# Kernel optimization log

Measured on AMD Instinct MI355X. Metric: run time of the kernel, lower is better.

The kernel has to match this reference:

```python
import jax, jax.numpy as jnp
import numpy as np
from jax import lax


def _maxpool_same(x, k):
    # stride-1 max pool with symmetric padding p=(k-1)//2, pad value -inf
    # (matches torch max_pool2d implicit -inf padding)
    p = (k - 1) // 2
    return lax.reduce_window(
        x,
        -jnp.inf,
        lax.max,
        window_dimensions=(1, 1, k, k),
        window_strides=(1, 1, 1, 1),
        padding=[(0, 0), (0, 0), (p, p), (p, p)],
    )


def setup_inputs() -> dict:
    key = jax.random.key(0)
    x = jax.random.normal(key, (16, 256, 64, 64), dtype=jnp.float32)
    return {"x": x}


def reference(x):
    # SPP: concat(x, maxpool5(x), maxpool9(x), maxpool13(x)) along channels
    x1 = _maxpool_same(x, 5)
    x2 = _maxpool_same(x, 9)
    x3 = _maxpool_same(x, 13)
    return jnp.concatenate([x, x1, x2, x3], axis=1)  # [B, 4C, H, W]
```

## Files before the change

### kernel.cpp

```cpp
#include <hip/hip_runtime.h>
#include <math.h>

#define TPB 256
#define W 64
#define H 64
#define LDSW 68

typedef float f32x4 __attribute__((ext_vector_type(4)));

__device__ __forceinline__ f32x4 max4(f32x4 a, f32x4 b) {
    f32x4 r;
    r.x = fmaxf(a.x, b.x); r.y = fmaxf(a.y, b.y);
    r.z = fmaxf(a.z, b.z); r.w = fmaxf(a.w, b.w);
    return r;
}

__device__ __forceinline__ void lds_barrier() {
    asm volatile("s_waitcnt lgkmcnt(0)\n\ts_barrier" ::: "memory");
}

__device__ __forceinline__ void p1_rest(const f32x4 v[4], float* __restrict__ s,
                                        float* __restrict__ outimg, int tid) {
    const int  lane = tid & 63;
    const int  lm1 = (lane - 1) & 63;
    const int  lp1 = (lane + 1) & 63;
    const bool qlo = (lane & 15) == 0;
    const bool qhi = (lane & 15) == 15;
    const float NEG = -INFINITY;
    f32x4* o4 = (f32x4*)outimg;
    #pragma unroll
    for (int i = 0; i < 4; ++i) {
        const int idx = tid + TPB * i;
        f32x4 t = v[i];
        __builtin_nontemporal_store(t, o4 + idx);
        float e0 = __shfl(t.z, lm1, 64);
        float e1 = __shfl(t.w, lm1, 64);
        float e6 = __shfl(t.x, lp1, 64);
        float e7 = __shfl(t.y, lp1, 64);
        if (qlo) { e0 = NEG; e1 = NEG; }
        if (qhi) { e6 = NEG; e7 = NEG; }
        const float e2 = t.x, e3 = t.y, e4 = t.z, e5 = t.w;
        const float p0 = fmaxf(e0, e1), p1 = fmaxf(e1, e2), p2 = fmaxf(e2, e3);
        const float p3 = fmaxf(e3, e4), p4 = fmaxf(e4, e5), p5 = fmaxf(e5, e6);
        f32x4 r;
        r.x = fmaxf(fmaxf(p0, p2), e4);
        r.y = fmaxf(fmaxf(p1, p3), e5);
        r.z = fmaxf(fmaxf(p2, p4), e6);
        r.w = fmaxf(fmaxf(p3, p5), e7);
        const int y = idx >> 4;
        const int q = idx & 15;
        *(f32x4*)&s[y * LDSW + 4 * q] = r;
    }
}

__device__ __forceinline__ void p2(const float* __restrict__ s,
                                   float* __restrict__ outimg, int tid) {
    const float NEG = -INFINITY;
    const size_t pstr = (size_t)256 * H * W;
    const int g    = tid & 15;
    const int x0   = g << 2;
    const int y0   = (tid >> 4) << 2;
    const int lane = tid & 63;
    const int lm1  = (lane - 1) & 63;
    const int lp1  = (lane + 1) & 63;
    const bool qlo = (g == 0);
    const bool qhi = (g == 15);

    f32x4 cv[16];
    #pragma unroll
    for (int j = 0; j < 16; ++j) {
        const int y  = y0 - 6 + j;
        const int yc = y < 0 ? 0 : (y > 63 ? 63 : y);
        f32x4 v = *(const f32x4*)&s[yc * LDSW + x0];
        if (y < 0 || y > 63) v = (f32x4){NEG, NEG, NEG, NEG};
        cv[j] = v;
    }
    f32x4 m2[15], m4[13], m8[9];
    #pragma unroll
    for (int j = 0; j < 15; ++j) m2[j] = max4(cv[j], cv[j + 1]);
    #pragma unroll
    for (int j = 0; j < 13; ++j) m4[j] = max4(m2[j], m2[j + 2]);
    #pragma unroll
    for (int j = 0; j < 9;  ++j) m8[j] = max4(m4[j], m4[j + 4]);

    float* o5  = outimg +     pstr;
    float* o9  = outimg + 2 * pstr;
    float* o13 = outimg + 3 * pstr;
    #pragma unroll
    for (int i = 0; i < 4; ++i) {
        const f32x4 c5  = max4(m4[i + 4], cv[i + 8]);
        const f32x4 c9  = max4(m8[i + 2], cv[i + 10]);
        const f32x4 c13 = max4(max4(m8[i], m4[i + 8]), cv[i + 12]);

        __builtin_nontemporal_store(c5, (f32x4*)(o5 + (y0 + i) * W + x0));

        const float Lz = __shfl(c9.z, lm1, 64);
        const float Lw = __shfl(c9.w, lm1, 64);
        const float Rx = __shfl(c9.x, lp1, 64);
        const float Ry = __shfl(c9.y, lp1, 64);
        const f32x4 lh9 = qlo ? (f32x4){c9.x, c9.x, c9.x, c9.y}
                              : (f32x4){Lz, Lw, c9.x, c9.y};
        const f32x4 rh9 = qhi ? (f32x4){c9.z, c9.w, c9.w, c9.w}
                              : (f32x4){c9.z, c9.w, Rx, Ry};
        __builtin_nontemporal_store(max4(lh9, rh9), (f32x4*)(o9 + (y0 + i) * W + x0));

        f32x4 L13, R13;
        L13.x = __shfl(c13.x, lm1, 64); L13.y = __shfl(c13.y, lm1, 64);
        L13.z = __shfl(c13.z, lm1, 64); L13.w = __shfl(c13.w, lm1, 64);
        R13.x = __shfl(c13.x, lp1, 64); R13.y = __shfl(c13.y, lp1, 64);
        R13.z = __shfl(c13.z, lp1, 64); R13.w = __shfl(c13.w, lp1, 64);
        const f32x4 lh13 = qlo ? (f32x4){c13.x, c13.x, c13.x, c13.x} : L13;
        const f32x4 rh13 = qhi ? (f32x4){c13.w, c13.w, c13.w, c13.w} : R13;
        __builtin_nontemporal_store(max4(max4(lh13, c13), rh13),
                                    (f32x4*)(o13 + (y0 + i) * W + x0));
    }
}

__global__ __launch_bounds__(TPB, 2) void spp_kernel(const float* __restrict__ in,
                                                     float* __restrict__ out) {
    __shared__ __align__(16) float s_a[H * LDSW];
    __shared__ __align__(16) float s_b[H * LDSW];

    const int tid  = threadIdx.x;
    const int imgA = blockIdx.x * 2;
    const int imgB = imgA + 1;
    const size_t obaseA = (((size_t)(imgA >> 8)) * 1024 + (imgA & 255)) * (H * W);
    const size_t obaseB = (((size_t)(imgB >> 8)) * 1024 + (imgB & 255)) * (H * W);

    f32x4 va[4], vb[4];
    {
        const f32x4* inA = (const f32x4*)(in + (size_t)imgA * (H * W));
        const f32x4* inB = (const f32x4*)(in + (size_t)imgB * (H * W));
        #pragma unroll
        for (int i = 0; i < 4; ++i) va[i] = __builtin_nontemporal_load(inA + tid + TPB * i);
        #pragma unroll
        for (int i = 0; i < 4; ++i) vb[i] = __builtin_nontemporal_load(inB + tid + TPB * i);
    }
    p1_rest(va, s_a, out + obaseA, tid);
    lds_barrier();

    p2(s_a, out + obaseA, tid);
    p1_rest(vb, s_b, out + obaseB, tid);
    lds_barrier();

    p2(s_b, out + obaseB, tid);
}

extern "C" void kernel_launch(void* const* d_in, const int* in_sizes, int n_in,
                              void* d_out, int out_size, void* d_ws, size_t ws_size,
                              hipStream_t stream) {
    const float* x = (const float*)d_in[0];
    float* out = (float*)d_out;
    spp_kernel<<<dim3(2048), dim3(TPB), 0, stream>>>(x, out);
}
```

Measured before the change: 308.8 us.

## Drop LDS staging, load halo rows from global, use DPP lane shifts

The kernel no longer stages a horizontally pooled image in LDS. Each thread loads its 16 halo rows straight from global memory (relying on L1/L2 for the 4x redundant reads), applies the horizontal 5-wide max to each row with DPP row shifts, and builds the 9 and 13 windows by chaining the separable 5-window results. It launches one image per block instead of two, raises the occupancy hint to 3, and replaces ds_bpermute shuffles with DPP. This removes the LDS traffic and barriers, at the cost of redundant global loads and horizontal max work repeated on halo rows.

Result: no change. 309.7 us (+0.3%).

```diff
diff --git a/kernel.cpp b/kernel.cpp
--- a/kernel.cpp
+++ b/kernel.cpp
@@ -4,7 +4,6 @@
 #define TPB 256
 #define W 64
 #define H 64
-#define LDSW 68
 
 typedef float f32x4 __attribute__((ext_vector_type(4)));
 
@@ -15,89 +14,94 @@
     return r;
 }
 
-__device__ __forceinline__ void lds_barrier() {
-    asm volatile("s_waitcnt lgkmcnt(0)\n\ts_barrier" ::: "memory");
+__device__ __forceinline__ float dpp_shr1(float v) {
+    return __int_as_float(__builtin_amdgcn_update_dpp(
+        0, __float_as_int(v), 0x111, 0xf, 0xf, true));
+}
+__device__ __forceinline__ float dpp_shl1(float v) {
+    return __int_as_float(__builtin_amdgcn_update_dpp(
+        0, __float_as_int(v), 0x101, 0xf, 0xf, true));
 }
 
-__device__ __forceinline__ void p1_rest(const f32x4 v[4], float* __restrict__ s,
-                                        float* __restrict__ outimg, int tid) {
-    const int  lane = tid & 63;
-    const int  lm1 = (lane - 1) & 63;
-    const int  lp1 = (lane + 1) & 63;
-    const bool qlo = (lane & 15) == 0;
-    const bool qhi = (lane & 15) == 15;
-    const float NEG = -INFINITY;
-    f32x4* o4 = (f32x4*)outimg;
-    #pragma unroll
-    for (int i = 0; i < 4; ++i) {
-        const int idx = tid + TPB * i;
-        f32x4 t = v[i];
-        __builtin_nontemporal_store(t, o4 + idx);
-        float e0 = __shfl(t.z, lm1, 64);
-        float e1 = __shfl(t.w, lm1, 64);
-        float e6 = __shfl(t.x, lp1, 64);
-        float e7 = __shfl(t.y, lp1, 64);
-        if (qlo) { e0 = NEG; e1 = NEG; }
-        if (qhi) { e6 = NEG; e7 = NEG; }
-        const float e2 = t.x, e3 = t.y, e4 = t.z, e5 = t.w;
-        const float p0 = fmaxf(e0, e1), p1 = fmaxf(e1, e2), p2 = fmaxf(e2, e3);
-        const float p3 = fmaxf(e3, e4), p4 = fmaxf(e4, e5), p5 = fmaxf(e5, e6);
-        f32x4 r;
-        r.x = fmaxf(fmaxf(p0, p2), e4);
-        r.y = fmaxf(fmaxf(p1, p3), e5);
-        r.z = fmaxf(fmaxf(p2, p4), e6);
-        r.w = fmaxf(fmaxf(p3, p5), e7);
-        const int y = idx >> 4;
-        const int q = idx & 15;
-        *(f32x4*)&s[y * LDSW + 4 * q] = r;
-    }
-}
-
-__device__ __forceinline__ void p2(const float* __restrict__ s,
-                                   float* __restrict__ outimg, int tid) {
-    const float NEG = -INFINITY;
-    const size_t pstr = (size_t)256 * H * W;
-    const int g    = tid & 15;
-    const int x0   = g << 2;
-    const int y0   = (tid >> 4) << 2;
-    const int lane = tid & 63;
-    const int lm1  = (lane - 1) & 63;
-    const int lp1  = (lane + 1) & 63;
+__global__ __launch_bounds__(TPB, 3) void spp_kernel(const float* __restrict__ in,
+                                                     float* __restrict__ out) {
+    const int tid = threadIdx.x;
+    const int img = blockIdx.x;
+    const int g   = tid & 15;
+    const int h   = tid >> 4;
+    const int x0  = g << 2;
+    const int y0  = h << 2;
     const bool qlo = (g == 0);
     const bool qhi = (g == 15);
+    const float NEG = -INFINITY;
+    const f32x4 NEG4 = {NEG, NEG, NEG, NEG};
 
-    f32x4 cv[16];
+    const size_t pstr  = (size_t)256 * H * W;
+    const size_t obase = (((size_t)(img >> 8)) * 1024 + (img & 255)) * (size_t)(H * W);
+    const float* ibase = in + (size_t)img * (H * W);
+
+    f32x4 rw[16];
     #pragma unroll
     for (int j = 0; j < 16; ++j) {
         const int y  = y0 - 6 + j;
         const int yc = y < 0 ? 0 : (y > 63 ? 63 : y);
-        f32x4 v = *(const f32x4*)&s[yc * LDSW + x0];
-        if (y < 0 || y > 63) v = (f32x4){NEG, NEG, NEG, NEG};
-        cv[j] = v;
+        rw[j] = *(const f32x4*)(ibase + yc * W + x0);
     }
-    f32x4 m2[15], m4[13], m8[9];
     #pragma unroll
-    for (int j = 0; j < 15; ++j) m2[j] = max4(cv[j], cv[j + 1]);
+    for (int j = 0; j < 16; ++j) {
+        const int y = y0 - 6 + j;
+        if (y < 0 || y > 63) rw[j] = NEG4;
+    }
+
+    float* o0 = out + obase;
     #pragma unroll
-    for (int j = 0; j < 13; ++j) m4[j] = max4(m2[j], m2[j + 2]);
+    for (int i = 0; i < 4; ++i)
+        __builtin_nontemporal_store(rw[6 + i], (f32x4*)(o0 + (y0 + i) * W + x0));
+
     #pragma unroll
-    for (int j = 0; j < 9;  ++j) m8[j] = max4(m4[j], m4[j + 4]);
+    for (int j = 0; j < 16; ++j) {
+        const f32x4 t = rw[j];
+        float e0 = dpp_shr1(t.z), e1 = dpp_shr1(t.w);
+        float e6 = dpp_shl1(t.x), e7 = dpp_shl1(t.y);
+        if (qlo) { e0 = NEG; e1 = NEG; }
+        if (qhi) { e6 = NEG; e7 = NEG; }
+        const float p0 = fmaxf(e0, e1),  p1 = fmaxf(e1, t.x), p2 = fmaxf(t.x, t.y);
+        const float p3 = fmaxf(t.y, t.z), p4 = fmaxf(t.z, t.w), p5 = fmaxf(t.w, e6);
+        f32x4 r;
+        r.x = fmaxf(fmaxf(p0, p2), t.z);
+        r.y = fmaxf(fmaxf(p1, p3), t.w);
+        r.z = fmaxf(fmaxf(p2, p4), e6);
+        r.w = fmaxf(fmaxf(p3, p5), e7);
+        rw[j] = r;
+    }
 
-    float* o5  = outimg +     pstr;
-    float* o9  = outimg + 2 * pstr;
-    float* o13 = outimg + 3 * pstr;
+    f32x4 col5[12];
+    {
+        f32x4 m2a = max4(rw[0], rw[1]);
+        f32x4 m2b = max4(rw[1], rw[2]);
+        #pragma unroll
+        for (int t = 0; t < 12; ++t) {
+            const f32x4 m2c = max4(rw[t + 2], rw[t + 3]);
+            col5[t] = max4(max4(m2a, m2c), rw[t + 4]);
+            m2a = m2b; m2b = m2c;
+        }
+    }
+
+    float* o5  = out + obase +     pstr;
+    float* o9  = out + obase + 2 * pstr;
+    float* o13 = out + obase + 3 * pstr;
     #pragma unroll
     for (int i = 0; i < 4; ++i) {
-        const f32x4 c5  = max4(m4[i + 4], cv[i + 8]);
-        const f32x4 c9  = max4(m8[i + 2], cv[i + 10]);
-        const f32x4 c13 = max4(max4(m8[i], m4[i + 8]), cv[i + 12]);
+        const f32x4 c5  = col5[i + 4];
+        const f32x4 c9  = max4(col5[i + 2], col5[i + 6]);
+        const f32x4 c13 = max4(max4(col5[i], col5[i + 4]), col5[i + 8]);
 
         __builtin_nontemporal_store(c5, (f32x4*)(o5 + (y0 + i) * W + x0));
 
-        const float Lz = __shfl(c9.z, lm1, 64);
-        const float Lw = __shfl(c9.w, lm1, 64);
-        const float Rx = __shfl(c9.x, lp1, 64);
-        const float Ry = __shfl(c9.y, lp1, 64);
+        const float Lz = dpp_shr1(c9.z);
+        const float Lw = dpp_shr1(c9.w);
+        const float Rx = dpp_shl1(c9.x);
+        const float Ry = dpp_shl1(c9.y);
         const f32x4 lh9 = qlo ? (f32x4){c9.x, c9.x, c9.x, c9.y}
                               : (f32x4){Lz, Lw, c9.x, c9.y};
         const f32x4 rh9 = qhi ? (f32x4){c9.z, c9.w, c9.w, c9.w}
@@ -105,10 +109,10 @@
         __builtin_nontemporal_store(max4(lh9, rh9), (f32x4*)(o9 + (y0 + i) * W + x0));
 
         f32x4 L13, R13;
-        L13.x = __shfl(c13.x, lm1, 64); L13.y = __shfl(c13.y, lm1, 64);
-        L13.z = __shfl(c13.z, lm1, 64); L13.w = __shfl(c13.w, lm1, 64);
-        R13.x = __shfl(c13.x, lp1, 64); R13.y = __shfl(c13.y, lp1, 64);
-        R13.z = __shfl(c13.z, lp1, 64); R13.w = __shfl(c13.w, lp1, 64);
+        L13.x = dpp_shr1(c13.x); L13.y = dpp_shr1(c13.y);
+        L13.z = dpp_shr1(c13.z); L13.w = dpp_shr1(c13.w);
+        R13.x = dpp_shl1(c13.x); R13.y = dpp_shl1(c13.y);
+        R13.z = dpp_shl1(c13.z); R13.w = dpp_shl1(c13.w);
         const f32x4 lh13 = qlo ? (f32x4){c13.x, c13.x, c13.x, c13.x} : L13;
         const f32x4 rh13 = qhi ? (f32x4){c13.w, c13.w, c13.w, c13.w} : R13;
         __builtin_nontemporal_store(max4(max4(lh13, c13), rh13),
@@ -116,40 +120,10 @@
     }
 }
 
-__global__ __launch_bounds__(TPB, 2) void spp_kernel(const float* __restrict__ in,
-                                                     float* __restrict__ out) {
-    __shared__ __align__(16) float s_a[H * LDSW];
-    __shared__ __align__(16) float s_b[H * LDSW];
-
-    const int tid  = threadIdx.x;
-    const int imgA = blockIdx.x * 2;
-    const int imgB = imgA + 1;
-    const size_t obaseA = (((size_t)(imgA >> 8)) * 1024 + (imgA & 255)) * (H * W);
-    const size_t obaseB = (((size_t)(imgB >> 8)) * 1024 + (imgB & 255)) * (H * W);
-
-    f32x4 va[4], vb[4];
-    {
-        const f32x4* inA = (const f32x4*)(in + (size_t)imgA * (H * W));
-        const f32x4* inB = (const f32x4*)(in + (size_t)imgB * (H * W));
-        #pragma unroll
-        for (int i = 0; i < 4; ++i) va[i] = __builtin_nontemporal_load(inA + tid + TPB * i);
-        #pragma unroll
-        for (int i = 0; i < 4; ++i) vb[i] = __builtin_nontemporal_load(inB + tid + TPB * i);
-    }
-    p1_rest(va, s_a, out + obaseA, tid);
-    lds_barrier();
-
-    p2(s_a, out + obaseA, tid);
-    p1_rest(vb, s_b, out + obaseB, tid);
-    lds_barrier();
-
-    p2(s_b, out + obaseB, tid);
-}
-
 extern "C" void kernel_launch(void* const* d_in, const int* in_sizes, int n_in,
                               void* d_out, int out_size, void* d_ws, size_t ws_size,
                               hipStream_t stream) {
     const float* x = (const float*)d_in[0];
     float* out = (float*)d_out;
-    spp_kernel<<<dim3(2048), dim3(TPB), 0, stream>>>(x, out);
+    spp_kernel<<<dim3(4096), dim3(TPB), 0, stream>>>(x, out);
 }
```
